# Optimization experiments

Measured on AMD Instinct MI355X. Metric: run time of the kernel, lower is better.

Reference implementation:

```python
import jax, jax.numpy as jnp
import numpy as np

NUM_HEADS = 16

def setup_inputs() -> dict:
    key = jax.random.key(0)
    k1, k2, k3 = jax.random.split(key, 3)
    T, B, E = 2048, 4, 1024
    x = jax.random.normal(k1, (T, B, E), dtype=jnp.float32)
    # xavier-ish scale for weights
    in_proj_w = jax.random.normal(k2, (3 * E, E), dtype=jnp.float32) * (1.0 / np.sqrt(E))
    in_proj_b = jnp.zeros((3 * E,), dtype=jnp.float32)
    out_w = jax.random.normal(k3, (E, E), dtype=jnp.float32) * (1.0 / np.sqrt(E))
    out_b = jnp.zeros((E,), dtype=jnp.float32)
    return {"x": x, "in_proj_w": in_proj_w, "in_proj_b": in_proj_b, "out_w": out_w, "out_b": out_b}

def reference(x, in_proj_w, in_proj_b, out_w, out_b):
    # Self-attention (qkv_same path), dropout=0, eval mode, no masks.
    T, B, E = x.shape
    H = NUM_HEADS
    Dh = E // H
    scaling = Dh ** (-0.5)
    # fused in-projection: [T,B,3E]
    qkv = jnp.einsum('tbe,fe->tbf', x, in_proj_w) + in_proj_b
    q, k, v = jnp.split(qkv, 3, axis=-1)
    q = q * scaling
    # [T,B,E] -> [B,H,T,Dh]
    def to_heads(t):
        return t.reshape(T, B, H, Dh).transpose(1, 2, 0, 3)
    q, k, v = to_heads(q), to_heads(k), to_heads(v)
    # full TxT score matrix, softmax in float32 (matches F.softmax(..., dtype=float32))
    scores = jnp.einsum('bhtd,bhsd->bhts', q, k)
    attn_weights = jax.nn.softmax(scores.astype(jnp.float32), axis=-1).astype(scores.dtype)
    attn = jnp.einsum('bhts,bhsd->bhtd', attn_weights, v)
    # [B,H,T,Dh] -> [T,B,E]
    attn = attn.transpose(2, 0, 1, 3).reshape(T, B, E)
    attn = jnp.einsum('tbe,fe->tbf', attn, out_w) + out_b
    # need_weights=True: average over heads -> [B,T,T]
    avg_weights = attn_weights.sum(axis=1) / H
    return attn, avg_weights
```

## Files before the change

### kernel.cpp

```cpp
#include <hip/hip_runtime.h>
#include <stdint.h>

#define DEV __device__ __forceinline__

typedef __attribute__((ext_vector_type(8))) __bf16 bf16x8;
typedef __attribute__((ext_vector_type(4))) __bf16 bf16x4;
typedef __attribute__((ext_vector_type(4))) float f32x4;

DEV unsigned short f2bf(float f){
  union { float fv; unsigned u; } v; v.fv = f;
  unsigned r = v.u + 0x7fffu + ((v.u >> 16) & 1u);
  return (unsigned short)(r >> 16);
}

DEV void gload16(const void* g, void* l){
  __builtin_amdgcn_global_load_lds((const __attribute__((address_space(1))) void*)g,
                                   (__attribute__((address_space(3))) void*)l,
                                   16, 0, 0);
}

__global__ void k_cvt(const float* __restrict__ src, unsigned short* __restrict__ dst){
  const int i = (blockIdx.x * blockDim.x + threadIdx.x) << 2;
  const float4 v = *(const float4*)(src + i);
  ushort4 o;
  o.x = f2bf(v.x); o.y = f2bf(v.y); o.z = f2bf(v.z); o.w = f2bf(v.w);
  *(ushort4*)(dst + i) = o;
}

template<int MODE>
__launch_bounds__(256, 2)
__global__ void k_gemm(const unsigned short* __restrict__ A,
                       const unsigned short* __restrict__ Bm,
                       const float* __restrict__ bias,
                       float* __restrict__ outF,
                       unsigned short* __restrict__ Qm,
                       unsigned short* __restrict__ Km,
                       unsigned short* __restrict__ VTm)
{
  __shared__ unsigned short As[2][128*64];
  __shared__ unsigned short Bs[2][128*64];
  const int tid  = threadIdx.x;
  const int lane = tid & 63;
  const int wid  = tid >> 6;
  const int wr   = wid >> 1;
  const int wc   = wid & 1;
  const int l15  = lane & 15;
  const int l4   = lane >> 4;
  const int wg  = blockIdx.x;
  const int by  = (wg & 7)*8 + ((wg >> 3) & 7);
  const int bx  = wg >> 6;
  const int r0  = by * 128;
  const int c0  = bx * 128;

  f32x4 acc[4][4];
#pragma unroll
  for (int m = 0; m < 4; ++m)
#pragma unroll
    for (int n = 0; n < 4; ++n)
      acc[m][n] = (f32x4){0.f, 0.f, 0.f, 0.f};

  auto STAGE = [&](int buf, int kt){
    const int k0 = kt << 6;
#pragma unroll
    for (int i = 0; i < 4; ++i){
      const int s = i*256 + tid;
      const int row = s >> 3;
      const int cg = (s & 7) ^ (row & 7);
      gload16(A + (size_t)(r0 + row)*1024 + k0 + cg*8, (void*)(&As[buf][s*8]));
    }
#pragma unroll
    for (int i = 0; i < 4; ++i){
      const int s = i*256 + tid;
      const int row = s >> 3;
      const int cg = (s & 7) ^ (row & 7);
      gload16(Bm + (size_t)(c0 + row)*1024 + k0 + cg*8, (void*)(&Bs[buf][s*8]));
    }
  };

  auto COMPUTE = [&](int buf){
#pragma unroll
    for (int kk = 0; kk < 2; ++kk){
      bf16x8 af[4], bf[4];
#pragma unroll
      for (int m = 0; m < 4; ++m){
        const int row = wr*64 + m*16 + l15;
        const int ch  = (kk*4 + l4) ^ (row & 7);
        af[m] = *(const bf16x8*)(&As[buf][row*64 + ch*8]);
      }
#pragma unroll
      for (int n = 0; n < 4; ++n){
        const int row = wc*64 + n*16 + l15;
        const int ch  = (kk*4 + l4) ^ (row & 7);
        bf[n] = *(const bf16x8*)(&Bs[buf][row*64 + ch*8]);
      }
      __builtin_amdgcn_s_setprio(1);
#pragma unroll
      for (int m = 0; m < 4; ++m)
#pragma unroll
        for (int n = 0; n < 4; ++n)
          acc[m][n] = __builtin_amdgcn_mfma_f32_16x16x32_bf16(af[m], bf[n], acc[m][n], 0, 0, 0);
      __builtin_amdgcn_s_setprio(0);
    }
  };

  STAGE(0, 0);
  for (int t = 0; t < 15; ++t){
    const int cur = t & 1;
    STAGE(cur ^ 1, t + 1);
    asm volatile("s_waitcnt vmcnt(8)" ::: "memory");
    asm volatile("s_barrier" ::: "memory");
    COMPUTE(cur);
    asm volatile("s_waitcnt lgkmcnt(0)" ::: "memory");
    asm volatile("s_barrier" ::: "memory");
  }
  asm volatile("s_waitcnt vmcnt(0)" ::: "memory");
  asm volatile("s_barrier" ::: "memory");
  COMPUTE(1);

  if (MODE == 0){
#pragma unroll
    for (int n = 0; n < 4; ++n){
      const int f     = c0 + wc*64 + n*16 + l15;
      const float bs  = bias[f];
      const int which = f >> 10;
      const int fi    = f & 1023;
      const int h     = fi >> 6;
      const int d     = fi & 63;
#pragma unroll
      for (int m = 0; m < 4; ++m){
        const int rb = r0 + wr*64 + m*16 + (l4 << 2);
#pragma unroll
        for (int j = 0; j < 4; ++j){
          const int r = rb + j;
          const int t = r >> 2;
          const int b = r & 3;
          float v = acc[m][n][j] + bs;
          if (which == 0) v *= 0.18033688f;
          const unsigned short bv = f2bf(v);
          const int bh = b*16 + h;
          if (which == 0)      Qm [((size_t)bh*2048 + t)*64 + d] = bv;
          else if (which == 1) Km [((size_t)bh*2048 + t)*64 + d] = bv;
          else                 VTm[((size_t)bh*64 + d)*2048 + t] = bv;
        }
      }
    }
  } else {
#pragma unroll
    for (int m = 0; m < 4; ++m){
      const int rb = r0 + wr*64 + m*16 + (l4 << 2);
#pragma unroll
      for (int n = 0; n < 4; ++n){
        const int f    = c0 + wc*64 + n*16 + l15;
        const float bs = bias[f];
#pragma unroll
        for (int j = 0; j < 4; ++j)
          outF[(size_t)(rb + j)*1024 + f] = acc[m][n][j] + bs;
      }
    }
  }
}

__launch_bounds__(512)
__global__ void k_pv(const unsigned short* __restrict__ Qm,
                     const unsigned short* __restrict__ Km,
                     const unsigned short* __restrict__ VTm,
                     float* __restrict__ linv,
                     unsigned short* __restrict__ ctx)
{
  __shared__ unsigned short Ws[256*64];
  __shared__ unsigned short Ks[2][64*64];
  __shared__ unsigned short Vs[2][64*64];
  const int tid = threadIdx.x, lane = tid & 63, wid = tid >> 6;
  const int l15 = lane & 15, l4 = lane >> 4;
  const int wg = blockIdx.x;
  const int slot = wg >> 3;
  const int bh = (wg & 7)*8 + (slot >> 3);
  const int t0 = (slot & 7) * 256;
  const unsigned short* Qb = Qm  + (size_t)bh*131072;
  const unsigned short* Kb = Km  + (size_t)bh*131072;
  const unsigned short* Vb = VTm + (size_t)bh*131072;

  {
    const int s = tid;
    const int row = s >> 3;
    const int cg = (s & 7) ^ (row & 7);
    gload16(Kb + (size_t)row*64 + cg*8, (void*)(Ks[0] + s*8));
    gload16(Vb + (size_t)row*2048 + cg*8, (void*)(Vs[0] + s*8));
  }
  bf16x8 aq[2][2];
#pragma unroll
  for (int qs = 0; qs < 2; ++qs)
#pragma unroll
    for (int kk = 0; kk < 2; ++kk)
      aq[qs][kk] = *(const bf16x8*)(Qb + (size_t)(t0 + wid*32 + qs*16 + l15)*64 + (kk*4 + l4)*8);
  __syncthreads();

  f32x4 oacc[2][4];
#pragma unroll
  for (int qs = 0; qs < 2; ++qs)
#pragma unroll
    for (int n = 0; n < 4; ++n) oacc[qs][n] = (f32x4){0.f,0.f,0.f,0.f};
  float lacc[2] = {0.f, 0.f};
  const int rx = l15 & 7;

  for (int s0 = 0; s0 < 2048; s0 += 64){
    const int cur = (s0 >> 6) & 1;
    if (s0 + 64 < 2048){
      const int s = tid;
      const int row = s >> 3;
      const int cg = (s & 7) ^ (row & 7);
      gload16(Kb + (size_t)(s0 + 64 + row)*64 + cg*8, (void*)(Ks[cur^1] + s*8));
      gload16(Vb + (size_t)row*2048 + (s0 + 64) + cg*8, (void*)(Vs[cur^1] + s*8));
    }
#pragma unroll
    for (int n = 0; n < 4; ++n){
      bf16x8 ak[2];
#pragma unroll
      for (int kk = 0; kk < 2; ++kk){
        const int ch = (kk*4 + l4) ^ rx;
        ak[kk] = *(const bf16x8*)(Ks[cur] + (n*16 + l15)*64 + ch*8);
      }
#pragma unroll
      for (int qs = 0; qs < 2; ++qs){
        f32x4 sacc = (f32x4){0.f,0.f,0.f,0.f};
        sacc = __builtin_amdgcn_mfma_f32_16x16x32_bf16(ak[0], aq[qs][0], sacc, 0, 0, 0);
        sacc = __builtin_amdgcn_mfma_f32_16x16x32_bf16(ak[1], aq[qs][1], sacc, 0, 0, 0);
        f32x4 pv;
        pv[0] = __builtin_amdgcn_exp2f(sacc[0]);
        pv[1] = __builtin_amdgcn_exp2f(sacc[1]);
        pv[2] = __builtin_amdgcn_exp2f(sacc[2]);
        pv[3] = __builtin_amdgcn_exp2f(sacc[3]);
        lacc[qs] += (pv[0] + pv[1]) + (pv[2] + pv[3]);
        const bf16x4 pb = __builtin_convertvector(pv, bf16x4);
        const int wrow = wid*32 + qs*16 + l15;
        const int g = (n*4 + l4) ^ (rx << 1);
        *(bf16x4*)(Ws + wrow*64 + g*4) = pb;
      }
    }
    bf16x8 aw[2][2];
#pragma unroll
    for (int qs = 0; qs < 2; ++qs)
#pragma unroll
      for (int kk = 0; kk < 2; ++kk){
        const int c = (kk*4 + l4) ^ rx;
        aw[qs][kk] = *(const bf16x8*)(Ws + (wid*32 + qs*16 + l15)*64 + c*8);
      }
#pragma unroll
    for (int n = 0; n < 4; ++n){
#pragma unroll
      for (int kk = 0; kk < 2; ++kk){
        const int ch = (kk*4 + l4) ^ rx;
        const bf16x8 bv = *(const bf16x8*)(Vs[cur] + (n*16 + l15)*64 + ch*8);
#pragma unroll
        for (int qs = 0; qs < 2; ++qs)
          oacc[qs][n] = __builtin_amdgcn_mfma_f32_16x16x32_bf16(aw[qs][kk], bv, oacc[qs][n], 0, 0, 0);
      }
    }
    __syncthreads();
  }

  const int b = bh >> 4, h = bh & 15;
#pragma unroll
  for (int qs = 0; qs < 2; ++qs){
    lacc[qs] += __shfl_xor(lacc[qs], 16);
    lacc[qs] += __shfl_xor(lacc[qs], 32);
    const float rl = 1.0f / lacc[qs];
    if (lane < 16)
      linv[(size_t)bh*2048 + t0 + wid*32 + qs*16 + lane] = rl;
    float rlj[4];
#pragma unroll
    for (int j = 0; j < 4; ++j)
      rlj[j] = __shfl(rl, (l4 << 2) + j);
#pragma unroll
    for (int n = 0; n < 4; ++n){
#pragma unroll
      for (int j = 0; j < 4; ++j){
        const int t = t0 + wid*32 + qs*16 + (l4 << 2) + j;
        const int d = n*16 + l15;
        ctx[((size_t)t*4 + b)*1024 + h*64 + d] = f2bf(oacc[qs][n][j] * rlj[j]);
      }
    }
  }
}

__launch_bounds__(256)
__global__ void k_avg(const unsigned short* __restrict__ Qm,
                      const unsigned short* __restrict__ Km,
                      const float* __restrict__ linv,
                      float* __restrict__ avg)
{
  __shared__ unsigned short Ks[2][128*64];
  const int tid = threadIdx.x, lane = tid & 63, wid = tid >> 6;
  const int l15 = lane & 15, l4 = lane >> 4;
  const int wg = blockIdx.x;
  const int slot = wg >> 3;
  const int combo = (wg & 7) + 8*(slot >> 4);
  const int b   = combo >> 4;
  const int s0  = (combo & 15) * 128;
  const int t0  = (slot & 15) * 128;
  const int rx  = l15 & 7;

  float wacc[2][8][4];
#pragma unroll
  for (int qs = 0; qs < 2; ++qs)
#pragma unroll
    for (int n = 0; n < 8; ++n)
#pragma unroll
      for (int j = 0; j < 4; ++j) wacc[qs][n][j] = 0.f;

  {
    const unsigned short* Kb = Km + (size_t)(b*16)*131072;
#pragma unroll
    for (int i = 0; i < 4; ++i){
      const int s = i*256 + tid;
      const int row = s >> 3;
      const int cg = (s & 7) ^ (row & 7);
      gload16(Kb + (size_t)(s0 + row)*64 + cg*8, (void*)(Ks[0] + s*8));
    }
  }

  for (int h = 0; h < 16; ++h){
    const int cur = h & 1;
    const int bh = b*16 + h;
    const unsigned short* Qb = Qm + (size_t)bh*131072;

    bf16x8 aq[2][2];
#pragma unroll
    for (int qs = 0; qs < 2; ++qs)
#pragma unroll
      for (int kk = 0; kk < 2; ++kk)
        aq[qs][kk] = *(const bf16x8*)(Qb + (size_t)(t0 + wid*32 + qs*16 + l15)*64 + (kk*4 + l4)*8);

    float4 lj[2];
#pragma unroll
    for (int qs = 0; qs < 2; ++qs){
      lj[qs] = *(const float4*)(linv + (size_t)bh*2048 + t0 + wid*32 + qs*16 + (l4 << 2));
      lj[qs].x *= 0.0625f; lj[qs].y *= 0.0625f; lj[qs].z *= 0.0625f; lj[qs].w *= 0.0625f;
    }

    if (h < 15){
      const unsigned short* Kb = Km + (size_t)(b*16 + h + 1)*131072;
#pragma unroll
      for (int i = 0; i < 4; ++i){
        const int s = i*256 + tid;
        const int row = s >> 3;
        const int cg = (s & 7) ^ (row & 7);
        gload16(Kb + (size_t)(s0 + row)*64 + cg*8, (void*)(Ks[cur^1] + s*8));
      }
      asm volatile("s_waitcnt vmcnt(4)" ::: "memory");
    } else {
      asm volatile("s_waitcnt vmcnt(0)" ::: "memory");
    }
    asm volatile("s_barrier" ::: "memory");

#pragma unroll
    for (int n = 0; n < 8; ++n){
      bf16x8 bk[2];
#pragma unroll
      for (int kk = 0; kk < 2; ++kk){
        const int ch = (kk*4 + l4) ^ rx;
        bk[kk] = *(const bf16x8*)(Ks[cur] + (n*16 + l15)*64 + ch*8);
      }
#pragma unroll
      for (int qs = 0; qs < 2; ++qs){
        f32x4 sacc = (f32x4){0.f,0.f,0.f,0.f};
        sacc = __builtin_amdgcn_mfma_f32_16x16x32_bf16(aq[qs][0], bk[0], sacc, 0, 0, 0);
        sacc = __builtin_amdgcn_mfma_f32_16x16x32_bf16(aq[qs][1], bk[1], sacc, 0, 0, 0);
        wacc[qs][n][0] += __builtin_amdgcn_exp2f(sacc[0]) * lj[qs].x;
        wacc[qs][n][1] += __builtin_amdgcn_exp2f(sacc[1]) * lj[qs].y;
        wacc[qs][n][2] += __builtin_amdgcn_exp2f(sacc[2]) * lj[qs].z;
        wacc[qs][n][3] += __builtin_amdgcn_exp2f(sacc[3]) * lj[qs].w;
      }
    }
    asm volatile("s_waitcnt lgkmcnt(0)" ::: "memory");
    asm volatile("s_barrier" ::: "memory");
  }

#pragma unroll
  for (int qs = 0; qs < 2; ++qs)
#pragma unroll
    for (int n = 0; n < 8; ++n)
#pragma unroll
      for (int j = 0; j < 4; ++j){
        const int t = t0 + wid*32 + qs*16 + (l4 << 2) + j;
        const int s = s0 + n*16 + l15;
        avg[((size_t)b*2048 + t)*2048 + s] = wacc[qs][n][j];
      }
}

extern "C" void kernel_launch(void* const* d_in, const int* in_sizes, int n_in,
                              void* d_out, int out_size, void* d_ws, size_t ws_size,
                              hipStream_t stream)
{
  const float* x    = (const float*)d_in[0];
  const float* wqkv = (const float*)d_in[1];
  const float* bqkv = (const float*)d_in[2];
  const float* wout = (const float*)d_in[3];
  const float* bout = (const float*)d_in[4];
  float* out = (float*)d_out;

  char* ws = (char*)d_ws;
  unsigned short* xb    = (unsigned short*)(ws);
  unsigned short* wqkvb = (unsigned short*)(ws + ((size_t)16 << 20));
  unsigned short* woutb = (unsigned short*)(ws + ((size_t)24 << 20));
  unsigned short* Qm    = (unsigned short*)(ws + ((size_t)26 << 20));
  unsigned short* Km    = (unsigned short*)(ws + ((size_t)42 << 20));
  unsigned short* VTm   = (unsigned short*)(ws + ((size_t)58 << 20));
  unsigned short* ctx   = (unsigned short*)(ws + ((size_t)74 << 20));
  float* linv = (float*)(ws + ((size_t)90 << 20));

  k_cvt<<<8192, 256, 0, stream>>>(x,    xb);
  k_cvt<<<3072, 256, 0, stream>>>(wqkv, wqkvb);
  k_cvt<<<1024, 256, 0, stream>>>(wout, woutb);

  k_gemm<0><<<1536, 256, 0, stream>>>(xb, wqkvb, bqkv, nullptr, Qm, Km, VTm);
  k_pv     <<< 512, 512, 0, stream>>>(Qm, Km, VTm, linv, ctx);
  k_avg    <<<1024, 256, 0, stream>>>(Qm, Km, linv, out + 8388608);
  k_gemm<1><<< 512, 256, 0, stream>>>(ctx, woutb, bout, out, nullptr, nullptr, nullptr);
}
```

Before: 275.0 us.

## Enlarge GEMM tiles to 256x128 with 8 waves and triple-buffered staging

The bf16 GEMM kernel now computes a 256x128 output tile per 512-thread block, with eight waves instead of four. Each B tile is reused across twice as many rows, which cuts global and L2 traffic per output. Staging moves from double to triple buffering, and each k-tile's loads are split in two halves interleaved with the two MFMA sub-steps, so more loads are in flight while compute runs. The cost is about 144KB of LDS per block, limiting occupancy to one block per CU. The grid also shrinks to 768 and 256 blocks, which can leave CUs unevenly loaded, especially for the output projection.

```diff
diff --git a/kernel.cpp b/kernel.cpp
--- a/kernel.cpp
+++ b/kernel.cpp
@@ -28,7 +28,7 @@
 }
 
 template<int MODE>
-__launch_bounds__(256, 2)
+__launch_bounds__(512, 1)
 __global__ void k_gemm(const unsigned short* __restrict__ A,
                        const unsigned short* __restrict__ Bm,
                        const float* __restrict__ bias,
@@ -37,8 +37,8 @@
                        unsigned short* __restrict__ Km,
                        unsigned short* __restrict__ VTm)
 {
-  __shared__ unsigned short As[2][128*64];
-  __shared__ unsigned short Bs[2][128*64];
+  __shared__ unsigned short As[3][256*64];
+  __shared__ unsigned short Bs[3][128*64];
   const int tid  = threadIdx.x;
   const int lane = tid & 63;
   const int wid  = tid >> 6;
@@ -47,9 +47,9 @@
   const int l15  = lane & 15;
   const int l4   = lane >> 4;
   const int wg  = blockIdx.x;
-  const int by  = (wg & 7)*8 + ((wg >> 3) & 7);
-  const int bx  = wg >> 6;
-  const int r0  = by * 128;
+  const int by  = (wg & 7)*4 + ((wg >> 3) & 3);
+  const int bx  = wg >> 5;
+  const int r0  = by * 256;
   const int c0  = bx * 128;
 
   f32x4 acc[4][4];
@@ -59,63 +59,62 @@
     for (int n = 0; n < 4; ++n)
       acc[m][n] = (f32x4){0.f, 0.f, 0.f, 0.f};
 
-  auto STAGE = [&](int buf, int kt){
-    const int k0 = kt << 6;
-#pragma unroll
-    for (int i = 0; i < 4; ++i){
-      const int s = i*256 + tid;
-      const int row = s >> 3;
-      const int cg = (s & 7) ^ (row & 7);
-      gload16(A + (size_t)(r0 + row)*1024 + k0 + cg*8, (void*)(&As[buf][s*8]));
-    }
-#pragma unroll
-    for (int i = 0; i < 4; ++i){
-      const int s = i*256 + tid;
-      const int row = s >> 3;
-      const int cg = (s & 7) ^ (row & 7);
-      gload16(Bm + (size_t)(c0 + row)*1024 + k0 + cg*8, (void*)(&Bs[buf][s*8]));
-    }
+  auto stageA = [&](int buf, int kt, int r){
+    const int s = r*512 + tid;
+    const int row = s >> 3;
+    const int cg = (s & 7) ^ (row & 7);
+    gload16(A + (size_t)(r0 + row)*1024 + (kt << 6) + cg*8, (void*)(&As[buf][s*8]));
   };
-
-  auto COMPUTE = [&](int buf){
-#pragma unroll
-    for (int kk = 0; kk < 2; ++kk){
-      bf16x8 af[4], bf[4];
-#pragma unroll
-      for (int m = 0; m < 4; ++m){
-        const int row = wr*64 + m*16 + l15;
-        const int ch  = (kk*4 + l4) ^ (row & 7);
-        af[m] = *(const bf16x8*)(&As[buf][row*64 + ch*8]);
-      }
-#pragma unroll
-      for (int n = 0; n < 4; ++n){
-        const int row = wc*64 + n*16 + l15;
-        const int ch  = (kk*4 + l4) ^ (row & 7);
-        bf[n] = *(const bf16x8*)(&Bs[buf][row*64 + ch*8]);
-      }
-      __builtin_amdgcn_s_setprio(1);
-#pragma unroll
-      for (int m = 0; m < 4; ++m)
-#pragma unroll
-        for (int n = 0; n < 4; ++n)
-          acc[m][n] = __builtin_amdgcn_mfma_f32_16x16x32_bf16(af[m], bf[n], acc[m][n], 0, 0, 0);
-      __builtin_amdgcn_s_setprio(0);
-    }
+  auto stageB = [&](int buf, int kt, int r){
+    const int s = r*512 + tid;
+    const int row = s >> 3;
+    const int cg = (s & 7) ^ (row & 7);
+    gload16(Bm + (size_t)(c0 + row)*1024 + (kt << 6) + cg*8, (void*)(&Bs[buf][s*8]));
   };
-
-  STAGE(0, 0);
-  for (int t = 0; t < 15; ++t){
-    const int cur = t & 1;
-    STAGE(cur ^ 1, t + 1);
-    asm volatile("s_waitcnt vmcnt(8)" ::: "memory");
+  auto stageH0 = [&](int kt){ const int b = kt % 3; stageA(b,kt,0); stageA(b,kt,1); stageB(b,kt,0); };
+  auto stageH1 = [&](int kt){ const int b = kt % 3; stageA(b,kt,2); stageA(b,kt,3); stageB(b,kt,1); };
+
+  auto compute_kk = [&](int buf, int kk){
+    bf16x8 af[4], bf[4];
+#pragma unroll
+    for (int m = 0; m < 4; ++m){
+      const int row = wr*64 + m*16 + l15;
+      const int ch  = (kk*4 + l4) ^ (row & 7);
+      af[m] = *(const bf16x8*)(&As[buf][row*64 + ch*8]);
+    }
+#pragma unroll
+    for (int n = 0; n < 4; ++n){
+      const int row = wc*64 + n*16 + l15;
+      const int ch  = (kk*4 + l4) ^ (row & 7);
+      bf[n] = *(const bf16x8*)(&Bs[buf][row*64 + ch*8]);
+    }
+    __builtin_amdgcn_s_setprio(1);
+#pragma unroll
+    for (int m = 0; m < 4; ++m)
+#pragma unroll
+      for (int n = 0; n < 4; ++n)
+        acc[m][n] = __builtin_amdgcn_mfma_f32_16x16x32_bf16(af[m], bf[n], acc[m][n], 0, 0, 0);
+    __builtin_amdgcn_s_setprio(0);
+  };
+
+  stageH0(0); stageH1(0);
+  stageH0(1); stageH1(1);
+  asm volatile("s_waitcnt vmcnt(6)" ::: "memory");
+  asm volatile("s_barrier" ::: "memory");
+
+  for (int t = 0; t < 16; ++t){
+    const int cur = t % 3;
+    if (t + 2 < 16) stageH0(t + 2);
+    if (t < 14)      { asm volatile("s_waitcnt vmcnt(9)" ::: "memory"); }
+    else if (t == 14){ asm volatile("s_waitcnt vmcnt(6)" ::: "memory"); }
+    else             { asm volatile("s_waitcnt vmcnt(0)" ::: "memory"); }
     asm volatile("s_barrier" ::: "memory");
-    COMPUTE(cur);
+    compute_kk(cur, 0);
+    if (t + 2 < 16) stageH1(t + 2);
+    compute_kk(cur, 1);
     asm volatile("s_waitcnt lgkmcnt(0)" ::: "memory");
     asm volatile("s_barrier" ::: "memory");
   }
-  asm volatile("s_waitcnt vmcnt(0)" ::: "memory");
-  asm volatile("s_barrier" ::: "memory");
-  COMPUTE(1);
 
   if (MODE == 0){
 #pragma unroll
@@ -413,8 +412,8 @@
   k_cvt<<<3072, 256, 0, stream>>>(wqkv, wqkvb);
   k_cvt<<<1024, 256, 0, stream>>>(wout, woutb);
 
-  k_gemm<0><<<1536, 256, 0, stream>>>(xb, wqkvb, bqkv, nullptr, Qm, Km, VTm);
-  k_pv     <<< 512, 512, 0, stream>>>(Qm, Km, VTm, linv, ctx);
+  k_gemm<0><<<768, 512, 0, stream>>>(xb, wqkvb, bqkv, nullptr, Qm, Km, VTm);
+  k_pv     <<<512, 512, 0, stream>>>(Qm, Km, VTm, linv, ctx);
   k_avg    <<<1024, 256, 0, stream>>>(Qm, Km, linv, out + 8388608);
-  k_gemm<1><<< 512, 256, 0, stream>>>(ctx, woutb, bout, out, nullptr, nullptr, nullptr);
-}
+  k_gemm<1><<<256, 512, 0, stream>>>(ctx, woutb, bout, out, nullptr, nullptr, nullptr);
+}
```

Measured after the change: 285.4 us. 3.8% more time.
